# Kernel tuning notes

Hardware: AMD Instinct MI355X
Metric: run time of the kernel (lower is better)

## Reference

```python
import jax, jax.numpy as jnp
import numpy as np

POND_MOD = 10000  # hardcoded modulus in the original forward


def setup_inputs() -> dict:
    key = jax.random.key(0)
    k1, k2, k3 = jax.random.split(key, 3)
    batch, seq_len, d_model = 4, 4096, 1024
    num_ponds, pond_capacity = 10, 10000
    context_vector = jax.random.normal(k1, (batch, seq_len, d_model), dtype=jnp.float32)
    pond_assignments = jax.random.randint(k2, (batch, seq_len), 0, num_ponds, dtype=jnp.int32)
    # stacked nn.Embedding weights: [num_ponds, pond_capacity, d_model]
    tables = jax.random.normal(k3, (num_ponds, pond_capacity, d_model), dtype=jnp.float32)
    return {"context_vector": context_vector, "pond_assignments": pond_assignments, "tables": tables}


def reference(context_vector, pond_assignments, tables):
    # per-token flavor index: int(abs(sum over d_model)) % 10000
    # int() truncates toward zero; value is non-negative after abs, so plain int cast matches.
    flavor = (jnp.abs(jnp.sum(context_vector, axis=-1)).astype(jnp.int32)) % POND_MOD  # [B, S]
    # gather the selected row from the selected pond's table, fully vectorized
    water_output = tables[pond_assignments, flavor]  # [B, S, d_model]
    return water_output
```

## Files before the change

kernel.cpp:

```cpp
#include <hip/hip_runtime.h>


#define POND_MOD 10000
#define D_MODEL  1024
#define PADDED   132
#define WAVE_LDS (8 * PADDED)

__global__ __launch_bounds__(256) void NeuralPonds_54898271977921_kernel(
    const float* __restrict__ ctx,
    const int*   __restrict__ pond,
    const float* __restrict__ tables,
    float*       __restrict__ out,
    int ntok)
{
    __shared__ float lds[4 * WAVE_LDS];

    const int lane  = threadIdx.x & 63;
    const int wid   = threadIdx.x >> 6;
    const int token = blockIdx.x * 4 + wid;
    const bool valid = token < ntok;
    const int  tok_safe = valid ? token : 0;

    const float4* row4 = (const float4*)(ctx + (size_t)tok_safe * D_MODEL);
    int pd = pond[tok_safe];
    float4 v[4];
    #pragma unroll
    for (int t = 0; t < 4; ++t)
        v[t] = row4[t * 64 + lane];

    float* w = lds + wid * WAVE_LDS;
    const int l31 = lane & 31;
    const int hb  = lane >> 5;
    #pragma unroll
    for (int t = 0; t < 4; ++t)
        *(float4*)(w + (2 * t + hb) * PADDED + 4 * l31) = v[t];

    __syncthreads();

    const int b = lane >> 3;
    const int j = lane & 7;
    const float* rp = w + b * PADDED + j;
    float r = rp[0];
    #pragma unroll
    for (int k = 1; k < 16; ++k)
        r += rp[8 * k];

    #pragma unroll
    for (int m = 1; m < 64; m <<= 1)
        r += __shfl_xor(r, m, 64);

    if (valid) {
        const int flavor = ((int)fabsf(r)) % POND_MOD;
        const float4* src = (const float4*)(tables + ((size_t)pd * POND_MOD + flavor) * D_MODEL);
        float4*       dst = (float4*)(out + (size_t)token * D_MODEL);
        #pragma unroll
        for (int k = 0; k < 4; ++k)
            dst[k * 64 + lane] = src[k * 64 + lane];
    }
}

extern "C" void kernel_launch(void* const* d_in, const int* in_sizes, int n_in,
                              void* d_out, int out_size, void* d_ws, size_t ws_size,
                              hipStream_t stream) {
    const float* ctx    = (const float*)d_in[0];
    const int*   pond   = (const int*)d_in[1];
    const float* tables = (const float*)d_in[2];
    float*       out    = (float*)d_out;

    const int ntok = in_sizes[1];
    const int blocks = (ntok + 3) / 4;

    NeuralPonds_54898271977921_kernel<<<blocks, 256, 0, stream>>>(
        ctx, pond, tables, out, ntok);
}
```

Measured before the change: 30.04 us.

## Split flavor reduction and row gather into separate kernels via workspace

Splits the fused kernel into a reduction kernel that writes per-token table row indices to the workspace and a gather kernel that copies rows using a wave-uniform index. Nontemporal load and store hints are added for the streamed context and output. A fused fallback without LDS runs when the workspace is too small. This decouples the gather from the reduction latency, at the cost of an extra launch and a full barrier between phases.

Result: faster. 27.85 us (median of 2 runs) (-7.3%).

```diff
diff --git a/kernel.cpp b/kernel.cpp
--- a/kernel.cpp
+++ b/kernel.cpp
@@ -6,11 +6,12 @@
 #define PADDED   132
 #define WAVE_LDS (8 * PADDED)
 
-__global__ __launch_bounds__(256) void NeuralPonds_54898271977921_kernel(
+typedef float f32x4 __attribute__((ext_vector_type(4)));
+
+__global__ __launch_bounds__(256) void np_flavor_kernel(
     const float* __restrict__ ctx,
     const int*   __restrict__ pond,
-    const float* __restrict__ tables,
-    float*       __restrict__ out,
+    int*         __restrict__ idxbuf,
     int ntok)
 {
     __shared__ float lds[4 * WAVE_LDS];
@@ -21,19 +22,19 @@
     const bool valid = token < ntok;
     const int  tok_safe = valid ? token : 0;
 
-    const float4* row4 = (const float4*)(ctx + (size_t)tok_safe * D_MODEL);
+    const f32x4* row4 = (const f32x4*)(ctx + (size_t)tok_safe * D_MODEL);
     int pd = pond[tok_safe];
-    float4 v[4];
+    f32x4 v[4];
     #pragma unroll
     for (int t = 0; t < 4; ++t)
-        v[t] = row4[t * 64 + lane];
+        v[t] = __builtin_nontemporal_load(&row4[t * 64 + lane]);
 
     float* w = lds + wid * WAVE_LDS;
     const int l31 = lane & 31;
     const int hb  = lane >> 5;
     #pragma unroll
     for (int t = 0; t < 4; ++t)
-        *(float4*)(w + (2 * t + hb) * PADDED + 4 * l31) = v[t];
+        *(f32x4*)(w + (2 * t + hb) * PADDED + 4 * l31) = v[t];
 
     __syncthreads();
 
@@ -49,14 +50,58 @@
     for (int m = 1; m < 64; m <<= 1)
         r += __shfl_xor(r, m, 64);
 
-    if (valid) {
+    if (valid && lane == 0) {
         const int flavor = ((int)fabsf(r)) % POND_MOD;
-        const float4* src = (const float4*)(tables + ((size_t)pd * POND_MOD + flavor) * D_MODEL);
-        float4*       dst = (float4*)(out + (size_t)token * D_MODEL);
-        #pragma unroll
-        for (int k = 0; k < 4; ++k)
-            dst[k * 64 + lane] = src[k * 64 + lane];
+        idxbuf[token] = pd * POND_MOD + flavor;
     }
+}
+
+__global__ __launch_bounds__(256) void np_gather_kernel(
+    const float* __restrict__ tables,
+    const int*   __restrict__ idxbuf,
+    float*       __restrict__ out,
+    int ntok)
+{
+    const int lane  = threadIdx.x & 63;
+    const int wid   = threadIdx.x >> 6;
+    const int token = blockIdx.x * 4 + wid;
+    if (token >= ntok) return;
+
+    const int idx = __builtin_amdgcn_readfirstlane(idxbuf[token]);
+    const f32x4* src = (const f32x4*)(tables + (size_t)idx * D_MODEL);
+    f32x4*       dst = (f32x4*)(out + (size_t)token * D_MODEL);
+
+    #pragma unroll
+    for (int k = 0; k < 4; ++k) {
+        f32x4 v = src[k * 64 + lane];
+        __builtin_nontemporal_store(v, &dst[k * 64 + lane]);
+    }
+}
+
+__global__ __launch_bounds__(256) void np_fused_kernel(
+    const float* __restrict__ ctx, const int* __restrict__ pond,
+    const float* __restrict__ tables, float* __restrict__ out, int ntok)
+{
+    const int lane  = threadIdx.x & 63;
+    const int wid   = threadIdx.x >> 6;
+    const int token = blockIdx.x * 4 + wid;
+    if (token >= ntok) return;
+
+    const float* row = ctx + (size_t)token * D_MODEL;
+    const int b = lane >> 3, j = lane & 7;
+    const float* p = row + b * 128 + j;
+    float r = p[0];
+    #pragma unroll
+    for (int k = 1; k < 16; ++k) r += p[8 * k];
+    #pragma unroll
+    for (int m = 1; m < 64; m <<= 1) r += __shfl_xor(r, m, 64);
+
+    const int flavor = ((int)fabsf(r)) % POND_MOD;
+    const int pd = pond[token];
+    const float4* src = (const float4*)(tables + ((size_t)pd * POND_MOD + flavor) * D_MODEL);
+    float4*       dst = (float4*)(out + (size_t)token * D_MODEL);
+    #pragma unroll
+    for (int k = 0; k < 4; ++k) dst[k * 64 + lane] = src[k * 64 + lane];
 }
 
 extern "C" void kernel_launch(void* const* d_in, const int* in_sizes, int n_in,
@@ -67,9 +112,14 @@
     const float* tables = (const float*)d_in[2];
     float*       out    = (float*)d_out;
 
-    const int ntok = in_sizes[1];
+    const int ntok   = in_sizes[1];
     const int blocks = (ntok + 3) / 4;
 
-    NeuralPonds_54898271977921_kernel<<<blocks, 256, 0, stream>>>(
-        ctx, pond, tables, out, ntok);
+    if (ws_size >= (size_t)ntok * sizeof(int)) {
+        int* idxbuf = (int*)d_ws;
+        np_flavor_kernel<<<blocks, 256, 0, stream>>>(ctx, pond, idxbuf, ntok);
+        np_gather_kernel<<<blocks, 256, 0, stream>>>(tables, idxbuf, out, ntok);
+    } else {
+        np_fused_kernel<<<blocks, 256, 0, stream>>>(ctx, pond, tables, out, ntok);
+    }
 }
```

## Process four tokens per wave with hoisted loads and nontemporal streaming

Applied to the files above, without the earlier changes.

Each wave now handles four tokens instead of one. All four context rows and pond indices are loaded up front so memory latency overlaps, and each token's reduction and gather then reuses double-buffered per-wave LDS regions. The block-wide __syncthreads is replaced by a wave-local lgkmcnt wait. Context loads and output stores use nontemporal hints to avoid polluting cache. The cost is higher register pressure (64 floats of context per lane) and a quarter as many blocks, which may reduce latency hiding across the GPU.

Result: slower. 30.85 us (+2.7%).

```diff
diff --git a/kernel.cpp b/kernel.cpp
--- a/kernel.cpp
+++ b/kernel.cpp
@@ -4,58 +4,112 @@
 #define POND_MOD 10000
 #define D_MODEL  1024
 #define PADDED   132
-#define WAVE_LDS (8 * PADDED)
+#define REGION   (8 * PADDED)
+#define TPW      4
 
-__global__ __launch_bounds__(256) void NeuralPonds_54898271977921_kernel(
+typedef float f32x4 __attribute__((ext_vector_type(4)));
+
+__global__ __launch_bounds__(256) void np_fused4_kernel(
     const float* __restrict__ ctx,
     const int*   __restrict__ pond,
     const float* __restrict__ tables,
     float*       __restrict__ out,
     int ntok)
 {
-    __shared__ float lds[4 * WAVE_LDS];
+    __shared__ float lds[4 * 2 * REGION];
 
-    const int lane  = threadIdx.x & 63;
-    const int wid   = threadIdx.x >> 6;
-    const int token = blockIdx.x * 4 + wid;
-    const bool valid = token < ntok;
-    const int  tok_safe = valid ? token : 0;
+    const int lane = threadIdx.x & 63;
+    const int wid  = threadIdx.x >> 6;
+    const int wave = blockIdx.x * 4 + wid;
+    const int base = wave * TPW;
+    if (base >= ntok) return;
+    const int cnt = (ntok - base) < TPW ? (ntok - base) : TPW;
 
-    const float4* row4 = (const float4*)(ctx + (size_t)tok_safe * D_MODEL);
-    int pd = pond[tok_safe];
-    float4 v[4];
-    #pragma unroll
-    for (int t = 0; t < 4; ++t)
-        v[t] = row4[t * 64 + lane];
-
-    float* w = lds + wid * WAVE_LDS;
     const int l31 = lane & 31;
     const int hb  = lane >> 5;
-    #pragma unroll
-    for (int t = 0; t < 4; ++t)
-        *(float4*)(w + (2 * t + hb) * PADDED + 4 * l31) = v[t];
+    const int b   = lane >> 3;
+    const int j   = lane & 7;
 
-    __syncthreads();
+    if (cnt == TPW) {
+        f32x4 v[TPW][4];
+        #pragma unroll
+        for (int i = 0; i < TPW; ++i) {
+            const f32x4* row4 = (const f32x4*)(ctx + (size_t)(base + i) * D_MODEL);
+            #pragma unroll
+            for (int t = 0; t < 4; ++t)
+                v[i][t] = __builtin_nontemporal_load(&row4[t * 64 + lane]);
+        }
+        int pd[TPW];
+        #pragma unroll
+        for (int i = 0; i < TPW; ++i)
+            pd[i] = pond[base + i];
 
-    const int b = lane >> 3;
-    const int j = lane & 7;
-    const float* rp = w + b * PADDED + j;
-    float r = rp[0];
-    #pragma unroll
-    for (int k = 1; k < 16; ++k)
-        r += rp[8 * k];
+        #pragma unroll
+        for (int i = 0; i < TPW; ++i) {
+            float* w = lds + (wid * 2 + (i & 1)) * REGION;
+            #pragma unroll
+            for (int t = 0; t < 4; ++t)
+                *(f32x4*)(w + (2 * t + hb) * PADDED + 4 * l31) = v[i][t];
 
-    #pragma unroll
-    for (int m = 1; m < 64; m <<= 1)
-        r += __shfl_xor(r, m, 64);
+            asm volatile("s_waitcnt lgkmcnt(0)" ::: "memory");
+            __builtin_amdgcn_sched_barrier(0);
 
-    if (valid) {
-        const int flavor = ((int)fabsf(r)) % POND_MOD;
-        const float4* src = (const float4*)(tables + ((size_t)pd * POND_MOD + flavor) * D_MODEL);
-        float4*       dst = (float4*)(out + (size_t)token * D_MODEL);
-        #pragma unroll
-        for (int k = 0; k < 4; ++k)
-            dst[k * 64 + lane] = src[k * 64 + lane];
+            const float* rp = w + b * PADDED + j;
+            float r = rp[0];
+            #pragma unroll
+            for (int k = 1; k < 16; ++k)
+                r += rp[8 * k];
+
+            #pragma unroll
+            for (int m = 1; m < 64; m <<= 1)
+                r += __shfl_xor(r, m, 64);
+
+            const int flavor = ((int)fabsf(r)) % POND_MOD;
+            const int idx    = pd[i] * POND_MOD + flavor;
+
+            const f32x4* src = (const f32x4*)(tables + (size_t)idx * D_MODEL);
+            f32x4*       dst = (f32x4*)(out + (size_t)(base + i) * D_MODEL);
+            #pragma unroll
+            for (int k = 0; k < 4; ++k) {
+                f32x4 g = src[k * 64 + lane];
+                __builtin_nontemporal_store(g, &dst[k * 64 + lane]);
+            }
+        }
+    } else {
+        for (int i = 0; i < cnt; ++i) {
+            const int token = base + i;
+            const f32x4* row4 = (const f32x4*)(ctx + (size_t)token * D_MODEL);
+            const int pdv = pond[token];
+            f32x4 v[4];
+            #pragma unroll
+            for (int t = 0; t < 4; ++t)
+                v[t] = row4[t * 64 + lane];
+
+            float* w = lds + (wid * 2 + (i & 1)) * REGION;
+            #pragma unroll
+            for (int t = 0; t < 4; ++t)
+                *(f32x4*)(w + (2 * t + hb) * PADDED + 4 * l31) = v[t];
+
+            asm volatile("s_waitcnt lgkmcnt(0)" ::: "memory");
+            __builtin_amdgcn_sched_barrier(0);
+
+            const float* rp = w + b * PADDED + j;
+            float r = rp[0];
+            #pragma unroll
+            for (int k = 1; k < 16; ++k)
+                r += rp[8 * k];
+            #pragma unroll
+            for (int m = 1; m < 64; m <<= 1)
+                r += __shfl_xor(r, m, 64);
+
+            const int flavor = ((int)fabsf(r)) % POND_MOD;
+            const int idx    = pdv * POND_MOD + flavor;
+            const f32x4* src = (const f32x4*)(tables + (size_t)idx * D_MODEL);
+            f32x4*       dst = (f32x4*)(out + (size_t)token * D_MODEL);
+            #pragma unroll
+            for (int k = 0; k < 4; ++k)
+                dst[k * 64 + lane] = src[k * 64 + lane];
+        }
     }
 }
 
@@ -67,9 +121,8 @@
     const float* tables = (const float*)d_in[2];
     float*       out    = (float*)d_out;
 
-    const int ntok = in_sizes[1];
-    const int blocks = (ntok + 3) / 4;
+    const int ntok   = in_sizes[1];
+    const int blocks = (ntok + 4 * TPW - 1) / (4 * TPW);
 
-    NeuralPonds_54898271977921_kernel<<<blocks, 256, 0, stream>>>(
-        ctx, pond, tables, out, ntok);
+    np_fused4_kernel<<<blocks, 256, 0, stream>>>(ctx, pond, tables, out, ntok);
 }
```
